# Kernel tuning notes

Measured on AMD Instinct MI355X. Metric: run time of the kernel, lower is better.

Reference implementation:

```python
import jax, jax.numpy as jnp
import numpy as np

N_NODES = 100000
N_EDGES = 3200000
IN_DIM, HID, N_LAB = 128, 64, 121


def setup_inputs() -> dict:
    key = jax.random.key(0)
    ks = jax.random.split(key, 8)
    x = jax.random.normal(ks[0], (N_NODES, IN_DIM), dtype=jnp.float32)
    edge_index = jax.random.randint(ks[1], (2, N_EDGES), 0, N_NODES, dtype=jnp.int64)
    W1 = jax.random.normal(ks[2], (IN_DIM, HID), dtype=jnp.float32) * (1.0 / np.sqrt(IN_DIM))
    b1 = jnp.zeros((HID,), dtype=jnp.float32)
    W2 = jax.random.normal(ks[3], (HID, HID), dtype=jnp.float32) * (1.0 / np.sqrt(HID))
    b2 = jnp.zeros((HID,), dtype=jnp.float32)
    Wout = jax.random.normal(ks[4], (HID, N_LAB), dtype=jnp.float32) * (1.0 / np.sqrt(HID))
    bout = jnp.zeros((N_LAB,), dtype=jnp.float32)
    return {"x": x, "edge_index": edge_index, "W1": W1, "b1": b1,
            "W2": W2, "b2": b2, "Wout": Wout, "bout": bout}


def _gcn_conv(x, W, b, src, dst, norm, n):
    # x' = D^{-1/2}(A+I)D^{-1/2} X W + b  (edges already include self-loops)
    xw = x @ W                                   # [N, out]
    msg = xw[src] * norm[:, None]                # [E+N, out] gather + scale
    agg = jax.ops.segment_sum(msg, dst, num_segments=n)  # scatter-add
    return agg + b


def reference(x, edge_index, W1, b1, W2, b2, Wout, bout):
    n = x.shape[0]
    loop = jnp.arange(n, dtype=edge_index.dtype)
    src = jnp.concatenate([edge_index[0], loop])
    dst = jnp.concatenate([edge_index[1], loop])
    # symmetric normalization (self-loops guarantee deg >= 1)
    deg = jax.ops.segment_sum(jnp.ones_like(dst, dtype=x.dtype), dst, num_segments=n)
    dinv = jax.lax.rsqrt(deg)
    norm = dinv[src] * dinv[dst]                 # [E+N]

    h = jax.nn.relu(_gcn_conv(x, W1, b1, src, dst, norm, n))
    # dropout p=0.5 is identity in eval mode (training=False)
    h = jax.nn.relu(_gcn_conv(h, W2, b2, src, dst, norm, n))
    logits = h @ Wout + bout                     # [N, num_labels]
    return logits
```

## Files before the change

### kernel.cpp

```cpp
#include <hip/hip_runtime.h>
#include <hip/hip_bf16.h>
#include <hip/hip_fp16.h>


#define IN_DIM 128
#define HID 64
#define N_LAB 121
#define NB_BLK 512

__global__ void scan1(const int* __restrict__ in, int* __restrict__ out,
                      int* __restrict__ bsums, int n) {
    __shared__ int s[256];
    int i = blockIdx.x * 256 + threadIdx.x;
    int v = (i < n) ? in[i] : 0;
    s[threadIdx.x] = v;
    __syncthreads();
    for (int off = 1; off < 256; off <<= 1) {
        int t = (threadIdx.x >= off) ? s[threadIdx.x - off] : 0;
        __syncthreads();
        s[threadIdx.x] += t;
        __syncthreads();
    }
    if (i < n) out[i] = s[threadIdx.x] - v;
    if (threadIdx.x == 255) bsums[blockIdx.x] = s[255];
}

__global__ __launch_bounds__(1024) void scan2(int* __restrict__ bsums, int nb) {
    __shared__ int s[1024];
    int v = (threadIdx.x < (unsigned)nb) ? bsums[threadIdx.x] : 0;
    s[threadIdx.x] = v;
    __syncthreads();
    for (int off = 1; off < 1024; off <<= 1) {
        int t = (threadIdx.x >= off) ? s[threadIdx.x - off] : 0;
        __syncthreads();
        s[threadIdx.x] += t;
        __syncthreads();
    }
    if (threadIdx.x < (unsigned)nb) bsums[threadIdx.x] = s[threadIdx.x] - v;
}

__global__ void scan_add(int* __restrict__ out, const int* __restrict__ bsums, int n) {
    int i = blockIdx.x * 256 + threadIdx.x;
    if (i < n) out[i] += bsums[blockIdx.x];
}

__global__ __launch_bounds__(256) void bucket_count(const int* __restrict__ dst,
                                                    int* __restrict__ counts,
                                                    int nbuk, int chunk, int E) {
    extern __shared__ int c[];
    for (int j = threadIdx.x; j < nbuk; j += 256) c[j] = 0;
    __syncthreads();
    int beg = blockIdx.x * chunk;
    int end = min(beg + chunk, E);
    for (int i = beg + threadIdx.x; i < end; i += 256)
        atomicAdd(&c[dst[i] >> 8], 1);
    __syncthreads();
    for (int j = threadIdx.x; j < nbuk; j += 256)
        counts[j * NB_BLK + blockIdx.x] = c[j];
}

__global__ __launch_bounds__(256) void bucket_scatter(const int* __restrict__ src,
                                                      const int* __restrict__ dst,
                                                      const int* __restrict__ base,
                                                      int* __restrict__ bucketed,
                                                      int nbuk, int chunk, int E) {
    extern __shared__ int c[];
    for (int j = threadIdx.x; j < nbuk; j += 256) c[j] = 0;
    __syncthreads();
    int beg = blockIdx.x * chunk;
    int end = min(beg + chunk, E);
    for (int i = beg + threadIdx.x; i < end; i += 256) {
        int d = dst[i];
        int b = d >> 8;
        int r = atomicAdd(&c[b], 1);
        int pos = base[b * NB_BLK + blockIdx.x] + r;
        bucketed[pos] = ((d & 255) << 17) | src[i];
    }
}

__global__ __launch_bounds__(256) void bucket_sort(const int* __restrict__ bucketed,
                                                   const int* __restrict__ base,
                                                   int* __restrict__ srcs,
                                                   int* __restrict__ row_ptr,
                                                   float* __restrict__ dinv,
                                                   int nbuk, int N, int E) {
    __shared__ int h[256];
    __shared__ int cur[256];
    int b = blockIdx.x;
    int nodeBase = b << 8;
    int s = base[b * NB_BLK];
    int e = (b == nbuk - 1) ? E : base[(b + 1) * NB_BLK];
    h[threadIdx.x] = 0;
    __syncthreads();
    for (int i = s + threadIdx.x; i < e; i += 256)
        atomicAdd(&h[bucketed[i] >> 17], 1);
    __syncthreads();
    int v = h[threadIdx.x];
    for (int off = 1; off < 256; off <<= 1) {
        int t = (threadIdx.x >= off) ? h[threadIdx.x - off] : 0;
        __syncthreads();
        h[threadIdx.x] += t;
        __syncthreads();
    }
    int excl = h[threadIdx.x] - v;
    cur[threadIdx.x] = excl;
    int node = nodeBase + threadIdx.x;
    if (node < N) {
        row_ptr[node] = s + excl;
        dinv[node] = rsqrtf((float)v + 1.0f);
    }
    if (b == nbuk - 1 && threadIdx.x == 0) row_ptr[N] = E;
    __syncthreads();
    for (int i = s + threadIdx.x; i < e; i += 256) {
        int p = bucketed[i];
        int d = p >> 17;
        int r = atomicAdd(&cur[d], 1);
        srcs[s + r] = (p & 0x1FFFF) << 7;
    }
}

template <int K, int N, typename OT>
__global__ __launch_bounds__(256) void gemm_kernel(
        const float* __restrict__ A, const float* __restrict__ B,
        const float* __restrict__ bias, const float* __restrict__ rowscale,
        OT* __restrict__ C, int M) {
    constexpr int ROWS = 64;
    constexpr int NPAD = (N <= 64) ? 64 : 128;
    constexpr int CG = NPAD / 4;
    constexpr int RG = 256 / CG;
    constexpr int RPT = ROWS / RG;
    __shared__ float Bs[K * NPAD];

    for (int i = threadIdx.x; i < K * NPAD; i += 256) {
        int c = i & (NPAD - 1);
        int k = i / NPAD;
        Bs[i] = (c < N) ? B[k * N + c] : 0.f;
    }
    __syncthreads();

    const int cg = threadIdx.x % CG;
    const int rg = threadIdx.x / CG;
    const int row_base = blockIdx.x * ROWS;

    const float* Arow[RPT];
    #pragma unroll
    for (int j = 0; j < RPT; ++j) {
        int r = row_base + rg + RG * j;
        if (r > M - 1) r = M - 1;
        Arow[j] = A + (size_t)r * K;
    }

    float acc[RPT][4];
    #pragma unroll
    for (int j = 0; j < RPT; ++j) {
        acc[j][0] = 0.f; acc[j][1] = 0.f; acc[j][2] = 0.f; acc[j][3] = 0.f;
    }

    for (int k = 0; k < K; k += 4) {
        float4 Bq[4];
        #pragma unroll
        for (int kk = 0; kk < 4; ++kk)
            Bq[kk] = *(const float4*)&Bs[(k + kk) * NPAD + cg * 4];
        #pragma unroll
        for (int j = 0; j < RPT; ++j) {
            const float4 Aq = *(const float4*)(Arow[j] + k);
            #pragma unroll
            for (int c = 0; c < 4; ++c) {
                const float b0 = ((const float*)&Bq[0])[c];
                const float b1 = ((const float*)&Bq[1])[c];
                const float b2 = ((const float*)&Bq[2])[c];
                const float b3 = ((const float*)&Bq[3])[c];
                float a = acc[j][c];
                a = fmaf(Aq.x, b0, a);
                a = fmaf(Aq.y, b1, a);
                a = fmaf(Aq.z, b2, a);
                a = fmaf(Aq.w, b3, a);
                acc[j][c] = a;
            }
        }
    }

    float bv[4];
    #pragma unroll
    for (int c = 0; c < 4; ++c) {
        int col = cg * 4 + c;
        bv[c] = (bias && col < N) ? bias[col] : 0.f;
    }

    #pragma unroll
    for (int j = 0; j < RPT; ++j) {
        const int r = row_base + rg + RG * j;
        if (r >= M) continue;
        const float sc = rowscale ? rowscale[r] : 1.0f;
        float o[4];
        #pragma unroll
        for (int c = 0; c < 4; ++c) o[c] = fmaf(acc[j][c], sc, bv[c]);
        OT* Crow = C + (size_t)r * N;
        if constexpr (sizeof(OT) == 4 && (N % 4 == 0)) {
            *(float4*)&Crow[cg * 4] = make_float4(o[0], o[1], o[2], o[3]);
        } else if constexpr (sizeof(OT) == 2 && (N % 4 == 0)) {
            __half2* p = (__half2*)&Crow[cg * 4];
            p[0] = __floats2half2_rn(o[0], o[1]);
            p[1] = __floats2half2_rn(o[2], o[3]);
        } else {
            #pragma unroll
            for (int c = 0; c < 4; ++c) {
                int col = cg * 4 + c;
                if (col < N) Crow[col] = (OT)o[c];
            }
        }
    }
}

__global__ __launch_bounds__(256) void aggregate(
        const __half* __restrict__ feat2, const int* __restrict__ rp,
        const int* __restrict__ srcs, const float* __restrict__ dinv,
        const float* __restrict__ bias, float* __restrict__ out, int N) {
    const int wid = (int)((((size_t)blockIdx.x * 256) + threadIdx.x) >> 6);
    if (wid >= N) return;
    const int lane = threadIdx.x & 63;
    const int slot = lane >> 3;
    const int oct  = lane & 7;
    const char* fbB = (const char*)feat2 + oct * 16;

    float acc[8];
    #pragma unroll
    for (int i = 0; i < 8; ++i) acc[i] = 0.f;

    if (slot == 0) {
        const uint4 q = *(const uint4*)(fbB + ((size_t)wid << 7));
        const __half2* h = (const __half2*)&q;
        #pragma unroll
        for (int i = 0; i < 4; ++i) {
            const float2 f = __half22float2(h[i]);
            acc[2 * i]     += f.x;
            acc[2 * i + 1] += f.y;
        }
    }

    const int beg = rp[wid], end = rp[wid + 1];
    int idx = beg + slot;
    while (__any(idx < end)) {
        const bool p0 = idx < end;
        const bool p1 = (idx + 8) < end;
        const int i0 = p0 ? idx : beg;
        const int i1 = p1 ? (idx + 8) : beg;
        const int o0 = srcs[i0];
        const int o1 = srcs[i1];
        uint4 q0 = *(const uint4*)(fbB + o0);
        uint4 q1 = *(const uint4*)(fbB + o1);
        if (!p0) { q0.x = 0u; q0.y = 0u; q0.z = 0u; q0.w = 0u; }
        if (!p1) { q1.x = 0u; q1.y = 0u; q1.z = 0u; q1.w = 0u; }
        const __half2* h0 = (const __half2*)&q0;
        const __half2* h1 = (const __half2*)&q1;
        #pragma unroll
        for (int i = 0; i < 4; ++i) {
            const float2 f0 = __half22float2(h0[i]);
            const float2 f1 = __half22float2(h1[i]);
            acc[2 * i]     += f0.x + f1.x;
            acc[2 * i + 1] += f0.y + f1.y;
        }
        idx += 16;
    }

    #pragma unroll
    for (int m = 8; m <= 32; m <<= 1) {
        #pragma unroll
        for (int i = 0; i < 8; ++i)
            acc[i] += __shfl_xor(acc[i], m, 64);
    }

    if (slot == 0) {
        const float sc = dinv[wid];
        float o[8];
        #pragma unroll
        for (int i = 0; i < 8; ++i)
            o[i] = fmaxf(fmaf(acc[i], sc, bias[oct * 8 + i]), 0.f);
        float4* d4 = (float4*)(out + (((size_t)wid << 6) + oct * 8));
        d4[0] = make_float4(o[0], o[1], o[2], o[3]);
        d4[1] = make_float4(o[4], o[5], o[6], o[7]);
    }
}

extern "C" void kernel_launch(void* const* d_in, const int* in_sizes, int n_in,
                              void* d_out, int out_size, void* d_ws, size_t ws_size,
                              hipStream_t stream) {
    const float* x    = (const float*)d_in[0];
    const int*   ei   = (const int*)d_in[1];
    const float* W1   = (const float*)d_in[2];
    const float* b1   = (const float*)d_in[3];
    const float* W2   = (const float*)d_in[4];
    const float* b2   = (const float*)d_in[5];
    const float* Wout = (const float*)d_in[6];
    const float* bout = (const float*)d_in[7];
    float* out = (float*)d_out;

    const int N = in_sizes[0] / IN_DIM;
    const int E = in_sizes[1] / 2;
    const int* srcI = ei;
    const int* dstI = ei + E;

    const int nbuk = (N + 255) >> 8;
    const int M1 = nbuk * NB_BLK;
    const int chunk = (E + NB_BLK - 1) / NB_BLK;

    int*    row_ptr = (int*)d_ws;
    float*  dinv    = (float*)(row_ptr + (N + 1));
    int*    counts  = (int*)(dinv + N);
    int*    base    = counts + M1;
    int*    bsums2  = base + M1;
    int*    srcs    = bsums2 + 1024;
    __half* feat2   = (__half*)(((uintptr_t)(srcs + E) + 15) & ~(uintptr_t)15);
    float*  hbuf    = (float*)(feat2 + (size_t)N * HID);
    int*    bucketed = (int*)feat2;

    const int nbM = (M1 + 255) / 256;
    const int gemmBlocks = (N + 63) / 64;
    const int aggBlocks = (int)(((size_t)N * HID + 255) / 256);
    const size_t ldsBuk = (size_t)nbuk * sizeof(int);

    bucket_count<<<NB_BLK, 256, ldsBuk, stream>>>(dstI, counts, nbuk, chunk, E);
    scan1<<<nbM, 256, 0, stream>>>(counts, base, bsums2, M1);
    scan2<<<1, 1024, 0, stream>>>(bsums2, nbM);
    scan_add<<<nbM, 256, 0, stream>>>(base, bsums2, M1);
    bucket_scatter<<<NB_BLK, 256, ldsBuk, stream>>>(srcI, dstI, base, bucketed, nbuk, chunk, E);
    bucket_sort<<<nbuk, 256, 0, stream>>>(bucketed, base, srcs, row_ptr, dinv, nbuk, N, E);

    gemm_kernel<IN_DIM, HID, __half><<<gemmBlocks, 256, 0, stream>>>(x, W1, nullptr, dinv, feat2, N);
    aggregate<<<aggBlocks, 256, 0, stream>>>(feat2, row_ptr, srcs, dinv, b1, hbuf, N);

    gemm_kernel<HID, HID, __half><<<gemmBlocks, 256, 0, stream>>>(hbuf, W2, nullptr, dinv, feat2, N);
    aggregate<<<aggBlocks, 256, 0, stream>>>(feat2, row_ptr, srcs, dinv, b2, hbuf, N);

    gemm_kernel<HID, N_LAB, float><<<gemmBlocks, 256, 0, stream>>>(hbuf, Wout, bout, nullptr, out, N);
}
```

Baseline: 511.3 us.

## Replace two-level bucket sort CSR build with global atomic counting sort

Replaces the bucketed two-pass CSR construction (per-block bucket counts, multi-level scan, bucket scatter, in-bucket sort) with a direct counting sort. It uses global atomic degree counts, a scan over nodes that also produces dinv, and an atomic-cursor scatter of source indices. It also raises the rows per block in the first two GEMMs to 128. This removes several kernels and an intermediate buffer pass, but relies on heavy global atomics and loses the deterministic, locality-friendly order of neighbours within each row.

Result: slower. 798.5 us (+56.2%).

```diff
diff --git a/kernel.cpp b/kernel.cpp
--- a/kernel.cpp
+++ b/kernel.cpp
@@ -6,13 +6,30 @@
 #define IN_DIM 128
 #define HID 64
 #define N_LAB 121
-#define NB_BLK 512
-
-__global__ void scan1(const int* __restrict__ in, int* __restrict__ out,
-                      int* __restrict__ bsums, int n) {
+
+__global__ void zero_int(int* __restrict__ p, int n) {
+    int i = blockIdx.x * 256 + threadIdx.x;
+    if (i < n) p[i] = 0;
+}
+
+__global__ __launch_bounds__(256) void deg_count(const int* __restrict__ dst,
+                                                 int* __restrict__ deg, int E) {
+    const int nPair = E >> 1;
+    const int2* d2 = (const int2*)dst;
+    for (int t = blockIdx.x * 256 + threadIdx.x; t < nPair; t += gridDim.x * 256) {
+        int2 d = d2[t];
+        atomicAdd(&deg[d.x], 1);
+        atomicAdd(&deg[d.y], 1);
+    }
+    if ((E & 1) && blockIdx.x == 0 && threadIdx.x == 0)
+        atomicAdd(&deg[dst[E - 1]], 1);
+}
+
+__global__ void scan1d(const int* __restrict__ deg, int* __restrict__ lexcl,
+                       int* __restrict__ bsums, float* __restrict__ dinv, int n) {
     __shared__ int s[256];
     int i = blockIdx.x * 256 + threadIdx.x;
-    int v = (i < n) ? in[i] : 0;
+    int v = (i < n) ? deg[i] : 0;
     s[threadIdx.x] = v;
     __syncthreads();
     for (int off = 1; off < 256; off <<= 1) {
@@ -21,110 +38,65 @@
         s[threadIdx.x] += t;
         __syncthreads();
     }
-    if (i < n) out[i] = s[threadIdx.x] - v;
+    if (i < n) {
+        lexcl[i] = s[threadIdx.x] - v;
+        dinv[i] = rsqrtf((float)v + 1.0f);
+    }
     if (threadIdx.x == 255) bsums[blockIdx.x] = s[255];
 }
 
-__global__ __launch_bounds__(1024) void scan2(int* __restrict__ bsums, int nb) {
-    __shared__ int s[1024];
+__global__ __launch_bounds__(512) void finalize_rp(const int* __restrict__ lexcl,
+                                                   const int* __restrict__ bsums,
+                                                   int* __restrict__ row_ptr,
+                                                   int* __restrict__ cur,
+                                                   int nb, int n, int E) {
+    __shared__ int s[512];
     int v = (threadIdx.x < (unsigned)nb) ? bsums[threadIdx.x] : 0;
     s[threadIdx.x] = v;
     __syncthreads();
-    for (int off = 1; off < 1024; off <<= 1) {
+    for (int off = 1; off < 512; off <<= 1) {
         int t = (threadIdx.x >= off) ? s[threadIdx.x - off] : 0;
         __syncthreads();
         s[threadIdx.x] += t;
         __syncthreads();
     }
-    if (threadIdx.x < (unsigned)nb) bsums[threadIdx.x] = s[threadIdx.x] - v;
-}
-
-__global__ void scan_add(int* __restrict__ out, const int* __restrict__ bsums, int n) {
-    int i = blockIdx.x * 256 + threadIdx.x;
-    if (i < n) out[i] += bsums[blockIdx.x];
-}
-
-__global__ __launch_bounds__(256) void bucket_count(const int* __restrict__ dst,
-                                                    int* __restrict__ counts,
-                                                    int nbuk, int chunk, int E) {
-    extern __shared__ int c[];
-    for (int j = threadIdx.x; j < nbuk; j += 256) c[j] = 0;
+    s[threadIdx.x] -= v;
     __syncthreads();
-    int beg = blockIdx.x * chunk;
-    int end = min(beg + chunk, E);
-    for (int i = beg + threadIdx.x; i < end; i += 256)
-        atomicAdd(&c[dst[i] >> 8], 1);
-    __syncthreads();
-    for (int j = threadIdx.x; j < nbuk; j += 256)
-        counts[j * NB_BLK + blockIdx.x] = c[j];
-}
-
-__global__ __launch_bounds__(256) void bucket_scatter(const int* __restrict__ src,
-                                                      const int* __restrict__ dst,
-                                                      const int* __restrict__ base,
-                                                      int* __restrict__ bucketed,
-                                                      int nbuk, int chunk, int E) {
-    extern __shared__ int c[];
-    for (int j = threadIdx.x; j < nbuk; j += 256) c[j] = 0;
-    __syncthreads();
-    int beg = blockIdx.x * chunk;
-    int end = min(beg + chunk, E);
-    for (int i = beg + threadIdx.x; i < end; i += 256) {
-        int d = dst[i];
-        int b = d >> 8;
-        int r = atomicAdd(&c[b], 1);
-        int pos = base[b * NB_BLK + blockIdx.x] + r;
-        bucketed[pos] = ((d & 255) << 17) | src[i];
-    }
-}
-
-__global__ __launch_bounds__(256) void bucket_sort(const int* __restrict__ bucketed,
-                                                   const int* __restrict__ base,
-                                                   int* __restrict__ srcs,
-                                                   int* __restrict__ row_ptr,
-                                                   float* __restrict__ dinv,
-                                                   int nbuk, int N, int E) {
-    __shared__ int h[256];
-    __shared__ int cur[256];
-    int b = blockIdx.x;
-    int nodeBase = b << 8;
-    int s = base[b * NB_BLK];
-    int e = (b == nbuk - 1) ? E : base[(b + 1) * NB_BLK];
-    h[threadIdx.x] = 0;
-    __syncthreads();
-    for (int i = s + threadIdx.x; i < e; i += 256)
-        atomicAdd(&h[bucketed[i] >> 17], 1);
-    __syncthreads();
-    int v = h[threadIdx.x];
-    for (int off = 1; off < 256; off <<= 1) {
-        int t = (threadIdx.x >= off) ? h[threadIdx.x - off] : 0;
-        __syncthreads();
-        h[threadIdx.x] += t;
-        __syncthreads();
-    }
-    int excl = h[threadIdx.x] - v;
-    cur[threadIdx.x] = excl;
-    int node = nodeBase + threadIdx.x;
-    if (node < N) {
-        row_ptr[node] = s + excl;
-        dinv[node] = rsqrtf((float)v + 1.0f);
-    }
-    if (b == nbuk - 1 && threadIdx.x == 0) row_ptr[N] = E;
-    __syncthreads();
-    for (int i = s + threadIdx.x; i < e; i += 256) {
-        int p = bucketed[i];
-        int d = p >> 17;
-        int r = atomicAdd(&cur[d], 1);
-        srcs[s + r] = (p & 0x1FFFF) << 7;
-    }
-}
-
-template <int K, int N, typename OT>
+    int i = blockIdx.x * 512 + threadIdx.x;
+    if (i < n) {
+        int rp = lexcl[i] + s[i >> 8];
+        row_ptr[i] = rp;
+        cur[i] = rp;
+    }
+    if (i == 0) row_ptr[n] = E;
+}
+
+__global__ __launch_bounds__(256) void scatter_edges(const int* __restrict__ src,
+                                                     const int* __restrict__ dst,
+                                                     int* __restrict__ cur,
+                                                     int* __restrict__ srcs, int E) {
+    const int nPair = E >> 1;
+    const int2* s2 = (const int2*)src;
+    const int2* d2 = (const int2*)dst;
+    for (int t = blockIdx.x * 256 + threadIdx.x; t < nPair; t += gridDim.x * 256) {
+        int2 d = d2[t];
+        int2 s = s2[t];
+        int p0 = atomicAdd(&cur[d.x], 1);
+        srcs[p0] = s.x << 7;
+        int p1 = atomicAdd(&cur[d.y], 1);
+        srcs[p1] = s.y << 7;
+    }
+    if ((E & 1) && blockIdx.x == 0 && threadIdx.x == 0) {
+        int p = atomicAdd(&cur[dst[E - 1]], 1);
+        srcs[p] = src[E - 1] << 7;
+    }
+}
+
+template <int K, int N, int ROWS, typename OT>
 __global__ __launch_bounds__(256) void gemm_kernel(
         const float* __restrict__ A, const float* __restrict__ B,
         const float* __restrict__ bias, const float* __restrict__ rowscale,
         OT* __restrict__ C, int M) {
-    constexpr int ROWS = 64;
     constexpr int NPAD = (N <= 64) ? 64 : 128;
     constexpr int CG = NPAD / 4;
     constexpr int RG = 256 / CG;
@@ -300,37 +272,36 @@
     const int* srcI = ei;
     const int* dstI = ei + E;
 
-    const int nbuk = (N + 255) >> 8;
-    const int M1 = nbuk * NB_BLK;
-    const int chunk = (E + NB_BLK - 1) / NB_BLK;
-
     int*    row_ptr = (int*)d_ws;
     float*  dinv    = (float*)(row_ptr + (N + 1));
-    int*    counts  = (int*)(dinv + N);
-    int*    base    = counts + M1;
-    int*    bsums2  = base + M1;
-    int*    srcs    = bsums2 + 1024;
+    int*    deg     = (int*)(dinv + N);
+    int*    lexcl   = deg + N;
+    int*    cur     = lexcl + N;
+    int*    bsums   = cur + N;
+    int*    srcs    = bsums + 512;
     __half* feat2   = (__half*)(((uintptr_t)(srcs + E) + 15) & ~(uintptr_t)15);
     float*  hbuf    = (float*)(feat2 + (size_t)N * HID);
-    int*    bucketed = (int*)feat2;
-
-    const int nbM = (M1 + 255) / 256;
-    const int gemmBlocks = (N + 63) / 64;
+
+    const int nbN  = (N + 255) / 256;
+    const int nbN2 = (N + 511) / 512;
+    const int gemmBlocks128 = (N + 127) / 128;
+    const int gemmBlocks64  = (N + 63) / 64;
     const int aggBlocks = (int)(((size_t)N * HID + 255) / 256);
-    const size_t ldsBuk = (size_t)nbuk * sizeof(int);
-
-    bucket_count<<<NB_BLK, 256, ldsBuk, stream>>>(dstI, counts, nbuk, chunk, E);
-    scan1<<<nbM, 256, 0, stream>>>(counts, base, bsums2, M1);
-    scan2<<<1, 1024, 0, stream>>>(bsums2, nbM);
-    scan_add<<<nbM, 256, 0, stream>>>(base, bsums2, M1);
-    bucket_scatter<<<NB_BLK, 256, ldsBuk, stream>>>(srcI, dstI, base, bucketed, nbuk, chunk, E);
-    bucket_sort<<<nbuk, 256, 0, stream>>>(bucketed, base, srcs, row_ptr, dinv, nbuk, N, E);
-
-    gemm_kernel<IN_DIM, HID, __half><<<gemmBlocks, 256, 0, stream>>>(x, W1, nullptr, dinv, feat2, N);
+
+    zero_int<<<nbN, 256, 0, stream>>>(deg, N);
+    deg_count<<<512, 256, 0, stream>>>(dstI, deg, E);
+    scan1d<<<nbN, 256, 0, stream>>>(deg, lexcl, bsums, dinv, N);
+    finalize_rp<<<nbN2, 512, 0, stream>>>(lexcl, bsums, row_ptr, cur, nbN, N, E);
+    scatter_edges<<<512, 256, 0, stream>>>(srcI, dstI, cur, srcs, E);
+
+    gemm_kernel<IN_DIM, HID, 128, __half><<<gemmBlocks128, 256, 0, stream>>>(
+        x, W1, nullptr, dinv, feat2, N);
     aggregate<<<aggBlocks, 256, 0, stream>>>(feat2, row_ptr, srcs, dinv, b1, hbuf, N);
 
-    gemm_kernel<HID, HID, __half><<<gemmBlocks, 256, 0, stream>>>(hbuf, W2, nullptr, dinv, feat2, N);
+    gemm_kernel<HID, HID, 128, __half><<<gemmBlocks128, 256, 0, stream>>>(
+        hbuf, W2, nullptr, dinv, feat2, N);
     aggregate<<<aggBlocks, 256, 0, stream>>>(feat2, row_ptr, srcs, dinv, b2, hbuf, N);
 
-    gemm_kernel<HID, N_LAB, float><<<gemmBlocks, 256, 0, stream>>>(hbuf, Wout, bout, nullptr, out, N);
-}
+    gemm_kernel<HID, N_LAB, 64, float><<<gemmBlocks64, 256, 0, stream>>>(
+        hbuf, Wout, bout, nullptr, out, N);
+}
```
